# Performance work log

Measured on AMD Instinct MI355X. Metric: run time of the kernel, lower is better.

Reference implementation:

```python
import jax, jax.numpy as jnp
import numpy as np

H = 16   # heads
M = 4    # stride / number of sparse slices


def setup_inputs() -> dict:
    key = jax.random.key(0)
    ks = jax.random.split(key, 5)
    B, L, D = 4, 4096, 1024
    s = 0.02
    return {
        "x": jax.random.normal(ks[0], (B, L, D), dtype=jnp.float32),
        "Wq": jax.random.normal(ks[1], (D, D), dtype=jnp.float32) * s,
        "bq": jnp.zeros((D,), dtype=jnp.float32),
        "Wk": jax.random.normal(ks[2], (D, D), dtype=jnp.float32) * s,
        "bk": jnp.zeros((D,), dtype=jnp.float32),
        "Wv": jax.random.normal(ks[3], (D, D), dtype=jnp.float32) * s,
        "bv": jnp.zeros((D,), dtype=jnp.float32),
        "Wo": jax.random.normal(ks[4], (D, D), dtype=jnp.float32) * s,
        "bo": jnp.zeros((D,), dtype=jnp.float32),
    }


def _strided_heads(y, B, L, D):
    # y: [B, L, D] -> [B, H, M, n, d_k] where slice m holds tokens m, m+M, m+2M, ...
    dk = D // H
    n = L // M
    y = y.reshape(B, L, H, dk).transpose(0, 2, 1, 3)          # [B,H,L,dk]
    y = y.reshape(B, H, n, M, dk).transpose(0, 1, 3, 2, 4)    # [B,H,M,n,dk]
    return y


def reference(x, Wq, bq, Wk, bk, Wv, bv, Wo, bo):
    B, L, D = x.shape
    dk = D // H
    n = L // M
    # projections (PyTorch Linear math: x @ W + b with W stored as [in, out] here)
    q = _strided_heads(x @ Wq + bq, B, L, D)   # [B,H,M,n,dk]
    k = _strided_heads(x @ Wk + bk, B, L, D)
    v = _strided_heads(x @ Wv + bv, B, L, D)
    # per-slice attention over the n strided tokens of each of the M slices
    scores = jnp.einsum("bhmqd,bhmkd->bhmqk", q, k) / jnp.sqrt(jnp.float32(dk))
    p = jax.nn.softmax(scores, axis=-1)
    o = jnp.einsum("bhmqk,bhmkd->bhmqd", p, v)                # [B,H,M,n,dk]
    # scatter back: slice m writes positions m::M  ==  interleave m and n dims
    o = o.transpose(0, 1, 3, 2, 4).reshape(B, H, L, dk)       # [B,H,L,dk]
    o = o.transpose(0, 2, 1, 3).reshape(B, L, D)              # [B,L,D]
    return o @ Wo + bo
```

## Files before the change

kernel.cpp:

```cpp
#include <hip/hip_runtime.h>
#include <hip/hip_bf16.h>


typedef __attribute__((ext_vector_type(8))) short short8;
typedef __attribute__((ext_vector_type(8))) unsigned short ushort8v;
typedef __attribute__((ext_vector_type(4))) float floatx4;

__device__ __forceinline__ float b2f(unsigned short h) {
    union { unsigned int u; float f; } v; v.u = ((unsigned int)h) << 16; return v.f;
}
__device__ __forceinline__ unsigned short f2b(float f) {
    union { float f; unsigned int u; } v; v.f = f;
    unsigned int r = v.u + 0x7fffu + ((v.u >> 16) & 1u);
    return (unsigned short)(r >> 16);
}
__device__ __forceinline__ unsigned int fbits(float f) {
    union { float f; unsigned int u; } v; v.f = f; return v.u;
}
__device__ __forceinline__ void async_copy16(const unsigned short* g, unsigned short* l) {
    __builtin_amdgcn_global_load_lds((const __attribute__((address_space(1))) void*)g,
                                     (__attribute__((address_space(3))) void*)l, 16, 0, 0);
}

__global__ __launch_bounds__(256)
void cvt_kernel(const float* __restrict__ in, unsigned short* __restrict__ out, int n4) {
    int i = blockIdx.x * 256 + threadIdx.x;
    if (i >= n4) return;
    float4 v = ((const float4*)in)[i];
    ushort4 o;
    o.x = f2b(v.x); o.y = f2b(v.y); o.z = f2b(v.z); o.w = f2b(v.w);
    ((ushort4*)out)[i] = o;
}

__global__ __launch_bounds__(256)
void cvt_w_t(const float* __restrict__ Wq, const float* __restrict__ Wk,
             const float* __restrict__ Wv, const float* __restrict__ Wo,
             unsigned short* __restrict__ Wt3, unsigned short* __restrict__ Wot, float s0) {
    __shared__ float tile[64][65];
    const int kt = blockIdx.x, nt = blockIdx.y, z = blockIdx.z;
    const float* W = (z == 0) ? Wq : (z == 1) ? Wk : (z == 2) ? Wv : Wo;
    unsigned short* Wt = (z < 3) ? (Wt3 + (size_t)z * 1048576) : Wot;
    const float sc = (z == 0) ? s0 : 1.0f;
    const int t = threadIdx.x;
    const int r = t >> 2, cg = t & 3;
    const float* src = W + (size_t)(kt * 64 + r) * 1024 + nt * 64 + cg * 16;
#pragma unroll
    for (int j = 0; j < 4; j++) {
        float4 v = *(const float4*)(src + j * 4);
        tile[r][cg * 16 + j * 4 + 0] = v.x;
        tile[r][cg * 16 + j * 4 + 1] = v.y;
        tile[r][cg * 16 + j * 4 + 2] = v.z;
        tile[r][cg * 16 + j * 4 + 3] = v.w;
    }
    __syncthreads();
    unsigned short* dst = Wt + (size_t)(nt * 64 + r) * 1024 + kt * 64 + cg * 16;
    ushort8v o0, o1;
#pragma unroll
    for (int j = 0; j < 8; j++) o0[j] = f2b(tile[cg * 16 + j][r] * sc);
#pragma unroll
    for (int j = 0; j < 8; j++) o1[j] = f2b(tile[cg * 16 + 8 + j][r] * sc);
    *(ushort8v*)(dst) = o0;
    *(ushort8v*)(dst + 8) = o1;
}

template <bool F32OUT>
__global__ __launch_bounds__(256, 2)
void gemm_k(const unsigned short* __restrict__ A,
            const unsigned short* __restrict__ BtBase,
            const float* __restrict__ bias0,
            const float* __restrict__ bias1,
            const float* __restrict__ bias2,
            void* __restrict__ OutBase, float s0) {
    constexpr int K = 1024, N = 1024;
    __shared__ __align__(16) unsigned short As[256 * 64];
    __shared__ __align__(16) unsigned short Bs[128 * 64];
    const int id = blockIdx.x;
    const int xcd = id & 7;
    const int q = id >> 3;
    const int tileM = xcd * 8 + (q & 7);
    const int rz = q >> 3;
    const int tileN = rz & 7;
    const int z = rz >> 3;
    const unsigned short* Bt = BtBase + (size_t)z * (1024 * 1024);
    const float* bias = (z == 0) ? bias0 : (z == 1 ? bias1 : bias2);
    const float bs = (z == 0) ? s0 : 1.0f;
    const int tid = threadIdx.x, w = tid >> 6, lane = tid & 63;
    const int wr = w >> 1, wc = w & 1;
    const int g = lane >> 4, c = lane & 15;
    const int c7 = c & 7;
    const int r8 = lane >> 3, j8 = lane & 7;
    const int kcs = (j8 ^ r8) * 8;

    floatx4 acc[8][4];
#pragma unroll
    for (int i = 0; i < 8; i++)
#pragma unroll
        for (int jj = 0; jj < 4; jj++) acc[i][jj] = (floatx4){0.f, 0.f, 0.f, 0.f};

    for (int kt = 0; kt < K / 64; ++kt) {
        __syncthreads();
#pragma unroll
        for (int t = 0; t < 8; t++) {
            int seg = w * 8 + t;
            int rowA = tileM * 256 + seg * 8 + r8;
            async_copy16(A + (size_t)rowA * K + kt * 64 + kcs, As + seg * 512);
        }
#pragma unroll
        for (int t = 0; t < 4; t++) {
            int seg = w * 4 + t;
            int rowB = tileN * 128 + seg * 8 + r8;
            async_copy16(Bt + (size_t)rowB * K + kt * 64 + kcs, Bs + seg * 512);
        }
        __syncthreads();
#pragma unroll
        for (int ks = 0; ks < 2; ks++) {
            const int kx = ((ks * 4 + g) ^ c7) * 8;
            short8 bf[4];
#pragma unroll
            for (int ct = 0; ct < 4; ct++)
                bf[ct] = *(const short8*)(Bs + (wc * 64 + ct * 16 + c) * 64 + kx);
#pragma unroll
            for (int rt = 0; rt < 8; rt++) {
                short8 af = *(const short8*)(As + (wr * 128 + rt * 16 + c) * 64 + kx);
#pragma unroll
                for (int ct = 0; ct < 4; ct++)
                    acc[rt][ct] = __builtin_amdgcn_mfma_f32_16x16x32_bf16(af, bf[ct], acc[rt][ct], 0, 0, 0);
            }
        }
    }
#pragma unroll
    for (int ct = 0; ct < 4; ct++) {
        int col = tileN * 128 + wc * 64 + ct * 16 + c;
        float bvv = bias[col] * bs;
#pragma unroll
        for (int rt = 0; rt < 8; rt++) {
            int row0 = tileM * 256 + wr * 128 + rt * 16 + g * 4;
#pragma unroll
            for (int r = 0; r < 4; r++) {
                float v = acc[rt][ct][r] + bvv;
                if (F32OUT) {
                    ((float*)OutBase)[(size_t)(row0 + r) * N + col] = v;
                } else {
                    ((unsigned short*)OutBase)[(size_t)z * (16384ull * 1024ull) +
                                               (size_t)(row0 + r) * N + col] = f2b(v);
                }
            }
        }
    }
}

__global__ __launch_bounds__(256)
void vtrans(const unsigned short* __restrict__ V, unsigned short* __restrict__ Vt) {
    __shared__ unsigned short tile[64 * 72];
    const int it = blockIdx.x, s = blockIdx.y;
    const int m = s & 3, h = (s >> 2) & 15, b = s >> 6;
    const int tid = threadIdx.x;
    {
        int il = tid >> 2, cg = tid & 3;
        const unsigned short* gsrc =
            V + ((size_t)b * 4096 + m + 4 * (it * 64 + il)) * 1024 + h * 64 + cg * 16;
        *(ushort8v*)(tile + il * 72 + cg * 16) = *(const ushort8v*)gsrc;
        *(ushort8v*)(tile + il * 72 + cg * 16 + 8) = *(const ushort8v*)(gsrc + 8);
    }
    __syncthreads();
    {
        int dl = tid >> 2, ig = (tid & 3) * 16;
        ushort8v o0, o1;
#pragma unroll
        for (int j = 0; j < 8; j++) o0[j] = tile[(ig + j) * 72 + dl];
#pragma unroll
        for (int j = 0; j < 8; j++) o1[j] = tile[(ig + 8 + j) * 72 + dl];
        unsigned short* dst = Vt + (size_t)s * 65536 + (size_t)dl * 1024 + it * 64 + ig;
        *(ushort8v*)dst = o0;
        *(ushort8v*)(dst + 8) = o1;
    }
}

__global__ __launch_bounds__(256, 4)
void attn_k(const unsigned short* __restrict__ Qg,
            const unsigned short* __restrict__ Kg,
            const unsigned short* __restrict__ Vt,
            unsigned short* __restrict__ Og) {
    __shared__ __align__(16) unsigned short Ks[64 * 64];
    __shared__ __align__(16) unsigned short Vs[64 * 64];
    __shared__ __align__(16) unsigned short Ps[4 * 2048];

    const int id = blockIdx.x;
    const int xcd = id & 7;
    const int qq = id >> 3;
    const int s = xcd * 32 + (qq >> 3);
    const int qt = qq & 7;
    const int m = s & 3, h = (s >> 2) & 15, b = s >> 6;
    const int tid = threadIdx.x, w = tid >> 6, lane = tid & 63;
    const int g = lane >> 4, c = lane & 15;
    const size_t rowBase = (size_t)b * 4096;

    short8 qf[2][2];
#pragma unroll
    for (int rt = 0; rt < 2; rt++)
#pragma unroll
        for (int ks = 0; ks < 2; ks++)
            qf[rt][ks] = *(const short8*)(Qg +
                (rowBase + (size_t)(m + 4 * (qt * 128 + w * 32 + rt * 16 + c))) * 1024 +
                h * 64 + ks * 32 + g * 8);

    const unsigned short* kPtr =
        Kg + (rowBase + (size_t)(m + 4 * (w * 16 + c))) * 1024 + h * 64 + g * 8;
    const unsigned short* vPtr =
        Vt + (size_t)s * 65536 + (size_t)(w * 16 + c) * 1024 + g * 8;

    short8 ones;
#pragma unroll
    for (int j = 0; j < 8; j++) ones[j] = (short)0x3F80;

    floatx4 oacc[2][4], lacc[2];
#pragma unroll
    for (int rt = 0; rt < 2; rt++) {
        lacc[rt] = (floatx4){0.f, 0.f, 0.f, 0.f};
#pragma unroll
        for (int dt = 0; dt < 4; dt++) oacc[rt][dt] = (floatx4){0.f, 0.f, 0.f, 0.f};
    }

    for (int kt = 0; kt < 16; ++kt) {
        __syncthreads();
        async_copy16(kPtr,      Ks + (w * 2 + 0) * 512);
        async_copy16(kPtr + 32, Ks + (w * 2 + 1) * 512);
        async_copy16(vPtr,      Vs + (w * 2 + 0) * 512);
        async_copy16(vPtr + 32, Vs + (w * 2 + 1) * 512);
        kPtr += 262144;
        vPtr += 64;
        __syncthreads();

        floatx4 sacc[4][2];
#pragma unroll
        for (int k4 = 0; k4 < 4; k4++)
#pragma unroll
            for (int rt = 0; rt < 2; rt++) sacc[k4][rt] = (floatx4){0.f, 0.f, 0.f, 0.f};
#pragma unroll
        for (int ks = 0; ks < 2; ks++) {
            short8 kf[4];
#pragma unroll
            for (int k4 = 0; k4 < 4; k4++)
                kf[k4] = *(const short8*)(Ks + (((k4 * 2 + ks) * 4 + g) * 16 + c) * 8);
#pragma unroll
            for (int k4 = 0; k4 < 4; k4++)
#pragma unroll
                for (int rt = 0; rt < 2; rt++)
                    sacc[k4][rt] = __builtin_amdgcn_mfma_f32_16x16x32_bf16(kf[k4], qf[rt][ks], sacc[k4][rt], 0, 0, 0);
        }

#pragma unroll
        for (int k4 = 0; k4 < 4; k4++) {
            const int kc = k4 >> 1;
            const int gr = (k4 & 1) * 2 + (g >> 1);
            const int j0 = (g & 1) * 4;
#pragma unroll
            for (int rt = 0; rt < 2; rt++) {
                unsigned int u0 = fbits(__builtin_amdgcn_exp2f(sacc[k4][rt][0])) + 0x8000u;
                unsigned int u1 = fbits(__builtin_amdgcn_exp2f(sacc[k4][rt][1])) + 0x8000u;
                unsigned int u2 = fbits(__builtin_amdgcn_exp2f(sacc[k4][rt][2])) + 0x8000u;
                unsigned int u3 = fbits(__builtin_amdgcn_exp2f(sacc[k4][rt][3])) + 0x8000u;
                uint2 pk;
                pk.x = __builtin_amdgcn_perm(u1, u0, 0x07060302u);
                pk.y = __builtin_amdgcn_perm(u3, u2, 0x07060302u);
                *(uint2*)(Ps + w * 2048 + (((rt * 2 + kc) * 4 + gr) * 16 + c) * 8 + j0) = pk;
            }
        }

#pragma unroll
        for (int kc = 0; kc < 2; kc++) {
            short8 pf[2], vf[4];
#pragma unroll
            for (int rt = 0; rt < 2; rt++)
                pf[rt] = *(const short8*)(Ps + w * 2048 + (((rt * 2 + kc) * 4 + g) * 16 + c) * 8);
#pragma unroll
            for (int dt = 0; dt < 4; dt++)
                vf[dt] = *(const short8*)(Vs + (((dt * 2 + kc) * 4 + g) * 16 + c) * 8);
#pragma unroll
            for (int rt = 0; rt < 2; rt++) {
                lacc[rt] = __builtin_amdgcn_mfma_f32_16x16x32_bf16(pf[rt], ones, lacc[rt], 0, 0, 0);
#pragma unroll
                for (int dt = 0; dt < 4; dt++)
                    oacc[rt][dt] = __builtin_amdgcn_mfma_f32_16x16x32_bf16(pf[rt], vf[dt], oacc[rt][dt], 0, 0, 0);
            }
        }
    }

#pragma unroll
    for (int rt = 0; rt < 2; rt++) {
#pragma unroll
        for (int r = 0; r < 4; r++) {
            float inv = 1.0f / lacc[rt][r];
            int token = m + 4 * (qt * 128 + w * 32 + rt * 16 + g * 4 + r);
            size_t rowOff = (rowBase + token) * 1024 + h * 64;
#pragma unroll
            for (int dt = 0; dt < 4; dt++)
                Og[rowOff + dt * 16 + c] = f2b(oacc[rt][dt][r] * inv);
        }
    }
}

extern "C" void kernel_launch(void* const* d_in, const int* in_sizes, int n_in,
                              void* d_out, int out_size, void* d_ws, size_t ws_size,
                              hipStream_t stream) {
    const float* x  = (const float*)d_in[0];
    const float* Wq = (const float*)d_in[1];
    const float* bq = (const float*)d_in[2];
    const float* Wk = (const float*)d_in[3];
    const float* bk = (const float*)d_in[4];
    const float* Wv = (const float*)d_in[5];
    const float* bv = (const float*)d_in[6];
    const float* Wo = (const float*)d_in[7];
    const float* bo = (const float*)d_in[8];

    const float SC = 0.18033688011112042f;

    char* ws = (char*)d_ws;
    const size_t SZ = 33554432;
    unsigned short* xb  = (unsigned short*)(ws);
    unsigned short* Vtp = (unsigned short*)(ws);
    unsigned short* qb  = (unsigned short*)(ws + SZ);
    unsigned short* ob  = (unsigned short*)(ws + 4 * SZ);
    unsigned short* Wt3 = (unsigned short*)(ws + 5 * SZ);
    unsigned short* Wot = Wt3 + 3ull * 1024 * 1024;

    cvt_kernel<<<16384, 256, 0, stream>>>(x, xb, 4194304);
    cvt_w_t<<<dim3(16, 16, 4), 256, 0, stream>>>(Wq, Wk, Wv, Wo, Wt3, Wot, SC);
    gemm_k<false><<<1536, 256, 0, stream>>>(xb, Wt3, bq, bk, bv, qb, SC);
    vtrans<<<dim3(16, 256), 256, 0, stream>>>(qb + 2ull * 16777216ull, Vtp);
    attn_k<<<2048, 256, 0, stream>>>(qb, qb + 16777216ull, Vtp, ob);
    gemm_k<true><<<512, 256, 0, stream>>>(ob, Wot, bo, bo, bo, d_out, 1.0f);
}
```

Baseline: 397.0 us.

## Double-buffer GEMM with 512-thread 256x256 tiles and interleaved async staging

The projection GEMM moves from 256x128 tiles with 4 waves to 256x256 tiles with 8 waves. LDS is now double-buffered, and next-stage A/B loads are issued asynchronously between MFMA phases, with explicit vmcnt waits, barriers and setprio. The goal is to hide global-load latency behind MFMA work and halve the B-tile reloads per output. The cost is double the LDS per block (128KB with launch_bounds(512,2)), which may limit occupancy, plus more fragile manual synchronization.

Result: slower. 424.4 us (+6.9%).

```diff
diff --git a/kernel.cpp b/kernel.cpp
--- a/kernel.cpp
+++ b/kernel.cpp
@@ -63,8 +63,30 @@
     *(ushort8v*)(dst + 8) = o1;
 }
 
+#define GEMM_PHASE(RT0, RT1, STAGE_STMT, TAILWAIT)                                                            \
+    {                                                                                                         \
+        short8 a0k0 = *(const short8*)(Ab + (RT0) * 1024 + kx0);                                              \
+        short8 a0k1 = *(const short8*)(Ab + (RT0) * 1024 + kx1);                                              \
+        short8 a1k0 = *(const short8*)(Ab + (RT1) * 1024 + kx0);                                              \
+        short8 a1k1 = *(const short8*)(Ab + (RT1) * 1024 + kx1);                                              \
+        STAGE_STMT                                                                                            \
+        __builtin_amdgcn_s_barrier();                                                                         \
+        __builtin_amdgcn_s_setprio(1);                                                                        \
+        _Pragma("unroll") for (int ct = 0; ct < 4; ct++)                                                      \
+            acc[RT0][ct] = __builtin_amdgcn_mfma_f32_16x16x32_bf16(a0k0, bfr[ct][0], acc[RT0][ct], 0, 0, 0);  \
+        _Pragma("unroll") for (int ct = 0; ct < 4; ct++)                                                      \
+            acc[RT1][ct] = __builtin_amdgcn_mfma_f32_16x16x32_bf16(a1k0, bfr[ct][0], acc[RT1][ct], 0, 0, 0);  \
+        _Pragma("unroll") for (int ct = 0; ct < 4; ct++)                                                      \
+            acc[RT0][ct] = __builtin_amdgcn_mfma_f32_16x16x32_bf16(a0k1, bfr[ct][1], acc[RT0][ct], 0, 0, 0);  \
+        _Pragma("unroll") for (int ct = 0; ct < 4; ct++)                                                      \
+            acc[RT1][ct] = __builtin_amdgcn_mfma_f32_16x16x32_bf16(a1k1, bfr[ct][1], acc[RT1][ct], 0, 0, 0);  \
+        __builtin_amdgcn_s_setprio(0);                                                                        \
+        TAILWAIT                                                                                              \
+        __builtin_amdgcn_s_barrier();                                                                         \
+    }
+
 template <bool F32OUT>
-__global__ __launch_bounds__(256, 2)
+__global__ __launch_bounds__(512, 2)
 void gemm_k(const unsigned short* __restrict__ A,
             const unsigned short* __restrict__ BtBase,
             const float* __restrict__ bias0,
@@ -72,24 +94,38 @@
             const float* __restrict__ bias2,
             void* __restrict__ OutBase, float s0) {
     constexpr int K = 1024, N = 1024;
-    __shared__ __align__(16) unsigned short As[256 * 64];
-    __shared__ __align__(16) unsigned short Bs[128 * 64];
+    __shared__ __align__(16) unsigned short As[2][16384];
+    __shared__ __align__(16) unsigned short Bs[2][16384];
     const int id = blockIdx.x;
     const int xcd = id & 7;
     const int q = id >> 3;
     const int tileM = xcd * 8 + (q & 7);
     const int rz = q >> 3;
-    const int tileN = rz & 7;
-    const int z = rz >> 3;
+    const int tileN = rz & 3;
+    const int z = rz >> 2;
     const unsigned short* Bt = BtBase + (size_t)z * (1024 * 1024);
     const float* bias = (z == 0) ? bias0 : (z == 1 ? bias1 : bias2);
     const float bs = (z == 0) ? s0 : 1.0f;
     const int tid = threadIdx.x, w = tid >> 6, lane = tid & 63;
-    const int wr = w >> 1, wc = w & 1;
+    const int wr = w >> 2, wc = w & 3;
     const int g = lane >> 4, c = lane & 15;
     const int c7 = c & 7;
     const int r8 = lane >> 3, j8 = lane & 7;
     const int kcs = (j8 ^ r8) * 8;
+    const int kx0 = ((g + 0) ^ c7) * 8;
+    const int kx1 = ((g + 4) ^ c7) * 8;
+
+    const unsigned short* aBase = A  + (size_t)(tileM * 256 + w * 16 + r8) * K + kcs;
+    const unsigned short* bBase = Bt + (size_t)(tileN * 256 + w * 16 + r8) * K + kcs;
+
+    auto stageA = [&](int kt, int h, int nb) {
+        async_copy16(aBase + (size_t)(h * 128) * K + kt * 64,     &As[nb][(h * 16 + w * 2 + 0) * 512]);
+        async_copy16(aBase + (size_t)(h * 128 + 8) * K + kt * 64, &As[nb][(h * 16 + w * 2 + 1) * 512]);
+    };
+    auto stageB = [&](int kt, int h, int nb) {
+        async_copy16(bBase + (size_t)(h * 128) * K + kt * 64,     &Bs[nb][(h * 16 + w * 2 + 0) * 512]);
+        async_copy16(bBase + (size_t)(h * 128 + 8) * K + kt * 64, &Bs[nb][(h * 16 + w * 2 + 1) * 512]);
+    };
 
     floatx4 acc[8][4];
 #pragma unroll
@@ -97,40 +133,36 @@
 #pragma unroll
         for (int jj = 0; jj < 4; jj++) acc[i][jj] = (floatx4){0.f, 0.f, 0.f, 0.f};
 
-    for (int kt = 0; kt < K / 64; ++kt) {
-        __syncthreads();
-#pragma unroll
-        for (int t = 0; t < 8; t++) {
-            int seg = w * 8 + t;
-            int rowA = tileM * 256 + seg * 8 + r8;
-            async_copy16(A + (size_t)rowA * K + kt * 64 + kcs, As + seg * 512);
-        }
-#pragma unroll
-        for (int t = 0; t < 4; t++) {
-            int seg = w * 4 + t;
-            int rowB = tileN * 128 + seg * 8 + r8;
-            async_copy16(Bt + (size_t)rowB * K + kt * 64 + kcs, Bs + seg * 512);
-        }
-        __syncthreads();
-#pragma unroll
-        for (int ks = 0; ks < 2; ks++) {
-            const int kx = ((ks * 4 + g) ^ c7) * 8;
-            short8 bf[4];
-#pragma unroll
-            for (int ct = 0; ct < 4; ct++)
-                bf[ct] = *(const short8*)(Bs + (wc * 64 + ct * 16 + c) * 64 + kx);
-#pragma unroll
-            for (int rt = 0; rt < 8; rt++) {
-                short8 af = *(const short8*)(As + (wr * 128 + rt * 16 + c) * 64 + kx);
-#pragma unroll
-                for (int ct = 0; ct < 4; ct++)
-                    acc[rt][ct] = __builtin_amdgcn_mfma_f32_16x16x32_bf16(af, bf[ct], acc[rt][ct], 0, 0, 0);
-            }
-        }
-    }
+    stageA(0, 0, 0); stageA(0, 1, 0);
+    stageB(0, 0, 0); stageB(0, 1, 0);
+    stageB(1, 0, 1); stageB(1, 1, 1);
+    asm volatile("s_waitcnt vmcnt(4)" ::: "memory");
+    __builtin_amdgcn_s_barrier();
+
+    for (int u = 0; u < 16; ++u) {
+        const int buf = u & 1;
+        const unsigned short* Ab = &As[buf][(wr * 128 + c) * 64];
+        const unsigned short* Bb = &Bs[buf][(wc * 64 + c) * 64];
+        short8 bfr[4][2];
+#pragma unroll
+        for (int ct = 0; ct < 4; ct++) {
+            bfr[ct][0] = *(const short8*)(Bb + ct * 1024 + kx0);
+            bfr[ct][1] = *(const short8*)(Bb + ct * 1024 + kx1);
+        }
+        GEMM_PHASE(0, 1, if (u + 1 < 16) { stageA(u + 1, 0, buf ^ 1); }, ;)
+        GEMM_PHASE(2, 3, if (u + 1 < 16) { stageA(u + 1, 1, buf ^ 1); }, ;)
+        GEMM_PHASE(4, 5, if (u + 2 < 16) { stageB(u + 2, 0, buf); }, ;)
+        if (u < 14) {
+            GEMM_PHASE(6, 7, { stageB(u + 2, 1, buf); },
+                       asm volatile("s_waitcnt vmcnt(4)" ::: "memory");)
+        } else {
+            GEMM_PHASE(6, 7, ;, asm volatile("s_waitcnt vmcnt(0)" ::: "memory");)
+        }
+    }
+
 #pragma unroll
     for (int ct = 0; ct < 4; ct++) {
-        int col = tileN * 128 + wc * 64 + ct * 16 + c;
+        int col = tileN * 256 + wc * 64 + ct * 16 + c;
         float bvv = bias[col] * bs;
 #pragma unroll
         for (int rt = 0; rt < 8; rt++) {
@@ -326,8 +358,8 @@
 
     cvt_kernel<<<16384, 256, 0, stream>>>(x, xb, 4194304);
     cvt_w_t<<<dim3(16, 16, 4), 256, 0, stream>>>(Wq, Wk, Wv, Wo, Wt3, Wot, SC);
-    gemm_k<false><<<1536, 256, 0, stream>>>(xb, Wt3, bq, bk, bv, qb, SC);
+    gemm_k<false><<<768, 512, 0, stream>>>(xb, Wt3, bq, bk, bv, qb, SC);
     vtrans<<<dim3(16, 256), 256, 0, stream>>>(qb + 2ull * 16777216ull, Vtp);
     attn_k<<<2048, 256, 0, stream>>>(qb, qb + 16777216ull, Vtp, ob);
-    gemm_k<true><<<512, 256, 0, stream>>>(ob, Wot, bo, bo, bo, d_out, 1.0f);
-}
+    gemm_k<true><<<256, 512, 0, stream>>>(ob, Wot, bo, bo, bo, d_out, 1.0f);
+}
```
